# Kernel optimization log

Hardware: AMD Instinct MI355X
Metric: run time of the kernel (lower is better)

## Reference

```python
import jax, jax.numpy as jnp
import numpy as np

N_NODES = 50000


def _gcn_conv(x, W, b, src, dst, n):
    """PyG GCNConv: add self-loops, symmetric normalization, sum-aggregate."""
    h = x @ W  # [N, out_dim] dense transform first (out_dim <= in_dim path)
    loop = jnp.arange(n, dtype=src.dtype)
    src_sl = jnp.concatenate([src, loop])
    dst_sl = jnp.concatenate([dst, loop])
    # degree computed on destination nodes (incl. self-loops)
    deg = jax.ops.segment_sum(jnp.ones_like(dst_sl, dtype=h.dtype), dst_sl, num_segments=n)
    dinv = jnp.where(deg > 0, jax.lax.rsqrt(deg), 0.0)
    norm = dinv[src_sl] * dinv[dst_sl]  # [E+N]
    msgs = h[src_sl] * norm[:, None]  # gather + scale, [E+N, out_dim]
    out = jax.ops.segment_sum(msgs, dst_sl, num_segments=n)  # scatter-add
    return out + b


def setup_inputs() -> dict:
    key = jax.random.key(0)
    k0, k1, k2, k3 = jax.random.split(key, 4)
    d = 256
    E = 400000
    scale = 1.0 / np.sqrt(d)
    x = jax.random.normal(k0, (N_NODES, d), dtype=jnp.float32)
    edge_index = jax.random.randint(k1, (2, E), 0, N_NODES, dtype=jnp.int64)
    W1 = jax.random.normal(k2, (d, d), dtype=jnp.float32) * scale
    b1 = jnp.zeros((d,), dtype=jnp.float32)
    W2 = jax.random.normal(k3, (d, d), dtype=jnp.float32) * scale
    b2 = jnp.zeros((d,), dtype=jnp.float32)
    return {"x": x, "edge_index": edge_index, "W1": W1, "b1": b1, "W2": W2, "b2": b2}


def reference(x, edge_index, W1, b1, W2, b2):
    src, dst = edge_index[0], edge_index[1]
    h = _gcn_conv(x, W1, b1, src, dst, N_NODES)
    h = jax.nn.relu(h)
    h = _gcn_conv(h, W2, b2, src, dst, N_NODES)
    h = jax.nn.relu(h)
    return h
```

## Files before the change

kernel.cpp:

```cpp
#include <hip/hip_runtime.h>
#include <stdint.h>

typedef __bf16 bf16_t;
typedef bf16_t bf16x4 __attribute__((ext_vector_type(4)));
typedef bf16_t bf16x8 __attribute__((ext_vector_type(8)));
typedef float f32x4 __attribute__((ext_vector_type(4)));

#define DIM 256
#define NNODES 50000

__device__ __forceinline__ int detect_f64(const int* __restrict__ ei) {
    int v = ei[2 * (threadIdx.x & 63) + 1];
    unsigned long long m = __ballot(v == 0);
    return __popcll(m) > 32;
}

__device__ __forceinline__ int load_edge(const int* __restrict__ ei, int E, int f64,
                                         int which , int e) {
    int v = f64 ? ei[(size_t)which * 2 * E + 2 * (size_t)e]
                : ei[(size_t)which * E + (size_t)e];
    return min(max(v, 0), NNODES - 1);
}

__global__ __launch_bounds__(256) void prep_kernel(int* __restrict__ counts,
                                                   const float* __restrict__ W1,
                                                   const float* __restrict__ W2,
                                                   bf16_t* __restrict__ Wf1,
                                                   bf16_t* __restrict__ Wf2, int n) {
    const int nb = (NNODES + 255) / 256;
    int b = blockIdx.x, t = threadIdx.x;
    if (b < nb) {
        int idx = b * 256 + t;
        if (idx < n) counts[idx] = 0;
    } else {
        int cw = b - nb;
        const float* W = (cw & 256) ? W2 : W1;
        bf16_t* Wf = (cw & 256) ? Wf2 : Wf1;
        int k = cw & 255;
        int s = k >> 5, quad = (k >> 3) & 3, j = k & 7;
        int nt = t >> 4, m = t & 15;
        Wf[s * 8192 + (nt * 64 + quad * 16 + m) * 8 + j] = (bf16_t)W[k * DIM + t];
    }
}

__global__ __launch_bounds__(256) void scan_kernel(const int* __restrict__ counts,
                                                   int* __restrict__ offsets,
                                                   int* __restrict__ cursor,
                                                   float* __restrict__ dinv, int n) {
    __shared__ int red[256];
    __shared__ int sm[256];
    int b = blockIdx.x, t = threadIdx.x;

    int part = 0;
    const int4* c4 = (const int4*)counts;
    int lim = b * 64;
    for (int j = t; j < lim; j += 256) {
        int4 v = c4[j];
        part += v.x + v.y + v.z + v.w;
    }
    red[t] = part;
    __syncthreads();
    #pragma unroll
    for (int off = 128; off > 0; off >>= 1) {
        if (t < off) red[t] += red[t + off];
        __syncthreads();
    }
    int base = red[0];

    int idx = b * 256 + t;
    int v = (idx < n) ? counts[idx] : 0;
    sm[t] = v;
    __syncthreads();
    #pragma unroll
    for (int off = 1; off < 256; off <<= 1) {
        int u = (t >= off) ? sm[t - off] : 0;
        __syncthreads();
        sm[t] += u;
        __syncthreads();
    }
    if (idx < n) {
        int incl = base + sm[t];
        offsets[idx + 1] = incl;
        cursor[idx] = incl - v;
        dinv[idx] = rsqrtf((float)(v + 1));
    }
    if (idx == 0) offsets[0] = 0;
}

__global__ void scatter_kernel(const int* __restrict__ ei, int E,
                               const float* __restrict__ dinv, int* __restrict__ cursor,
                               int2* __restrict__ csr_e) {
    int f64 = detect_f64(ei);
    int e = blockIdx.x * blockDim.x + threadIdx.x;
    if (e < E) {
        int s = load_edge(ei, E, f64, 0, e);
        int d = load_edge(ei, E, f64, 1, e);
        int pos = atomicAdd(&cursor[d], 1);
        if (pos >= 0 && pos < E) {
            int2 v;
            v.x = s;
            v.y = __float_as_int(dinv[s] * dinv[d]);
            csr_e[pos] = v;
        }
    }
}

#define SWROW 552

template <bool F32A>
__device__ __forceinline__ void gemm_body(const void* __restrict__ Xv,
                                          const bf16_t* __restrict__ Wf,
                                          bf16_t* __restrict__ H, int tiles, int bid,
                                          char* smem) {
    bf16_t* sB = (bf16_t*)smem;
    int tid = threadIdx.x;
    int wave = tid >> 6, lane = tid & 63;
    int m = lane & 15, quad = lane >> 4;
    int tile = bid * 4 + wave;
    bool active = tile < tiles;
    int arow = (min(tile, tiles - 1)) * 16 + m;

    f32x4 acc[16] = {};

    auto stage = [&](int s, int buf) {
        const char* g = (const char*)Wf + s * 16384 + wave * 4096 + lane * 16;
        char* l = smem + buf * 16384 + wave * 4096;
        #pragma unroll
        for (int it = 0; it < 4; it++) {
            __builtin_amdgcn_global_load_lds(
                (const __attribute__((address_space(1))) void*)(g + it * 1024),
                (__attribute__((address_space(3))) void*)(l + it * 1024), 16, 0, 0);
        }
    };

    stage(0, 0);
    __syncthreads();

    for (int s = 0; s < 8; s++) {
        int cur = s & 1;
        if (s < 7) stage(s + 1, cur ^ 1);

        bf16x8 a;
        if (F32A) {
            const f32x4* xp = (const f32x4*)((const float*)Xv + (size_t)arow * DIM + s * 32 + quad * 8);
            f32x4 x0 = xp[0], x1 = xp[1];
            #pragma unroll
            for (int j = 0; j < 4; j++) { a[j] = (bf16_t)x0[j]; a[j + 4] = (bf16_t)x1[j]; }
        } else {
            a = *(const bf16x8*)((const bf16_t*)Xv + (size_t)arow * DIM + s * 32 + quad * 8);
        }

        const bf16_t* bs = sB + cur * 8192;
        #pragma unroll
        for (int nt = 0; nt < 16; nt++) {
            bf16x8 b = *(const bf16x8*)(bs + nt * 512 + lane * 8);
            acc[nt] = __builtin_amdgcn_mfma_f32_16x16x32_bf16(a, b, acc[nt], 0, 0, 0);
        }

        __syncthreads();
    }

    char* sW = smem + wave * (16 * SWROW);
    #pragma unroll
    for (int nt = 0; nt < 16; nt++) {
        #pragma unroll
        for (int r = 0; r < 4; r++) {
            *(bf16_t*)(sW + (quad * 4 + r) * SWROW + (nt * 16 + m) * 2) = (bf16_t)acc[nt][r];
        }
    }
    if (active) {
        bf16_t* Hrow = H + (size_t)tile * 16 * DIM;
        #pragma unroll
        for (int j = 0; j < 16; j++) {
            bf16x4 v = *(const bf16x4*)(sW + j * SWROW + lane * 8);
            *(bf16x4*)(Hrow + j * DIM + lane * 4) = v;
        }
    }
}

__global__ __launch_bounds__(256, 4) void gemm1_hist_kernel(const float* __restrict__ X,
                                                            const bf16_t* __restrict__ Wf,
                                                            bf16_t* __restrict__ H, int tiles,
                                                            int gemm_blocks,
                                                            const int* __restrict__ ei, int E,
                                                            int* __restrict__ counts) {
    __shared__ char smem[4 * 16 * SWROW];
    if ((int)blockIdx.x >= gemm_blocks) {
        int f64 = detect_f64(ei);
        int e = (blockIdx.x - gemm_blocks) * 256 + threadIdx.x;
        if (e < E) atomicAdd(&counts[load_edge(ei, E, f64, 1, e)], 1);
        return;
    }
    gemm_body<true>(X, Wf, H, tiles, blockIdx.x, smem);
}

__global__ __launch_bounds__(256, 4) void gemm2_kernel(const bf16_t* __restrict__ Xv,
                                                       const bf16_t* __restrict__ Wf,
                                                       bf16_t* __restrict__ H, int tiles) {
    __shared__ char smem[4 * 16 * SWROW];
    gemm_body<false>(Xv, Wf, H, tiles, blockIdx.x, smem);
}

template <int OUT_BF16>
__global__ __launch_bounds__(256) void aggregate_kernel(const bf16_t* __restrict__ H,
                                                        const int* __restrict__ offsets,
                                                        const int2* __restrict__ csr_e,
                                                        const float* __restrict__ dinv,
                                                        const float* __restrict__ bias,
                                                        void* __restrict__ outv, int n) {
    int wg = threadIdx.x >> 5;
    int l = threadIdx.x & 31;
    int i = blockIdx.x * 8 + wg;
    if (i >= n) return;

    const char* Hb = (const char*)H;
    int doff = l * 16;

    auto cvt = [](bf16x4 v) -> f32x4 {
        f32x4 r;
        #pragma unroll
        for (int j = 0; j < 4; j++) r[j] = (float)v[j];
        return r;
    };
    auto lo4 = [](bf16x8 v) -> bf16x4 { return __builtin_shufflevector(v, v, 0, 1, 2, 3); };
    auto hi4 = [](bf16x8 v) -> bf16x4 { return __builtin_shufflevector(v, v, 4, 5, 6, 7); };

    float dii = dinv[i];
    bf16x8 selfv = *(const bf16x8*)(Hb + ((size_t)i << 9) + doff);
    f32x4 acc0 = cvt(lo4(selfv)) * (dii * dii);
    f32x4 acc1 = cvt(hi4(selfv)) * (dii * dii);

    int e0 = offsets[i], e1 = offsets[i + 1];
    int e = e0;
    for (; e + 8 <= e1; e += 8) {
        unsigned s[8]; float w[8];
        #pragma unroll
        for (int j = 0; j < 8; j++) {
            int2 t = csr_e[e + j];
            s[j] = min((unsigned)t.x, (unsigned)(NNODES - 1));
            w[j] = __int_as_float(t.y);
        }
        bf16x8 h[8];
        #pragma unroll
        for (int j = 0; j < 8; j++) {
            h[j] = *(const bf16x8*)(Hb + ((size_t)s[j] << 9) + doff);
        }
        __builtin_amdgcn_sched_barrier(0);
        #pragma unroll
        for (int j = 0; j < 8; j++) {
            acc0 += cvt(lo4(h[j])) * w[j];
            acc1 += cvt(hi4(h[j])) * w[j];
        }
    }
    if (e < e1) {
        bf16x8 z;
        #pragma unroll
        for (int q = 0; q < 8; q++) z[q] = (bf16_t)0.0f;
        unsigned s[8]; float w[8]; bool val[8];
        #pragma unroll
        for (int j = 0; j < 8; j++) {
            bool valid = (e + j) < e1;
            val[j] = valid;
            int2 t = csr_e[valid ? e + j : e];
            s[j] = min((unsigned)t.x, (unsigned)(NNODES - 1));
            w[j] = valid ? __int_as_float(t.y) : 0.0f;
        }
        bf16x8 h[8];
        #pragma unroll
        for (int j = 0; j < 8; j++) {
            h[j] = z;
            if (val[j]) h[j] = *(const bf16x8*)(Hb + ((size_t)s[j] << 9) + doff);
        }
        __builtin_amdgcn_sched_barrier(0);
        #pragma unroll
        for (int j = 0; j < 8; j++) {
            acc0 += cvt(lo4(h[j])) * w[j];
            acc1 += cvt(hi4(h[j])) * w[j];
        }
    }

    const f32x4* bp = (const f32x4*)(bias + l * 8);
    acc0 += bp[0];
    acc1 += bp[1];
    #pragma unroll
    for (int j = 0; j < 4; j++) {
        acc0[j] = fmaxf(acc0[j], 0.0f);
        acc1[j] = fmaxf(acc1[j], 0.0f);
    }

    if (OUT_BF16) {
        bf16x8 o;
        #pragma unroll
        for (int j = 0; j < 4; j++) { o[j] = (bf16_t)acc0[j]; o[j + 4] = (bf16_t)acc1[j]; }
        *(bf16x8*)((bf16_t*)outv + (size_t)i * DIM + l * 8) = o;
    } else {
        float* op = (float*)outv + (size_t)i * DIM + l * 8;
        *(f32x4*)op = acc0;
        *(f32x4*)(op + 4) = acc1;
    }
}


extern "C" void kernel_launch(void* const* d_in, const int* in_sizes, int n_in,
                              void* d_out, int out_size, void* d_ws, size_t ws_size,
                              hipStream_t stream) {
    const float* x  = (const float*)d_in[0];
    const int*   ei = (const int*)d_in[1];
    const float* W1 = (const float*)d_in[2];
    const float* b1 = (const float*)d_in[3];
    const float* W2 = (const float*)d_in[4];
    const float* b2 = (const float*)d_in[5];
    float* out = (float*)d_out;

    const int n = NNODES;
    const int E = in_sizes[1] / 2;
    const int nb = (n + 255) / 256;

    char* ws = (char*)d_ws;
    size_t off = 0;
    auto alloc = [&](size_t bytes) -> char* {
        char* p = ws + off;
        off += (bytes + 255) & ~(size_t)255;
        return p;
    };
    float*  dinv     = (float*)alloc((size_t)n * 4);
    int*    counts   = (int*)alloc((size_t)n * 4);
    int*    offsets  = (int*)alloc((size_t)(n + 1) * 4);
    int*    cursor   = (int*)alloc((size_t)n * 4);
    int2*   csr_e    = (int2*)alloc((size_t)E * 8);
    bf16_t* Wf1      = (bf16_t*)alloc((size_t)DIM * DIM * 2);
    bf16_t* Wf2      = (bf16_t*)alloc((size_t)DIM * DIM * 2);
    bf16_t* P        = (bf16_t*)alloc((size_t)n * DIM * 2);
    bf16_t* X2       = (bf16_t*)alloc((size_t)n * DIM * 2);

    int tiles = (n + 15) / 16;
    int gemm_blocks = (tiles + 3) / 4;
    int hist_blocks = (E + 255) / 256;
    int agg_blocks = (n + 7) / 8;

    prep_kernel<<<nb + 512, 256, 0, stream>>>(counts, W1, W2, Wf1, Wf2, n);
    gemm1_hist_kernel<<<gemm_blocks + hist_blocks, 256, 0, stream>>>(x, Wf1, P, tiles,
                                                                     gemm_blocks, ei, E, counts);
    scan_kernel<<<nb, 256, 0, stream>>>(counts, offsets, cursor, dinv, n);
    scatter_kernel<<<hist_blocks, 256, 0, stream>>>(ei, E, dinv, cursor, csr_e);
    aggregate_kernel<1><<<agg_blocks, 256, 0, stream>>>(P, offsets, csr_e, dinv, b1, X2, n);
    gemm2_kernel<<<gemm_blocks, 256, 0, stream>>>(X2, Wf2, P, tiles);
    aggregate_kernel<0><<<agg_blocks, 256, 0, stream>>>(P, offsets, csr_e, dinv, b2, out, n);
}
```

Before: 246.7 us.

## Fuse layer-1 aggregation with layer-2 GEMM via LDS-resident activations

Layer-1 aggregation now runs inside the layer-2 GEMM kernel. Each block gathers 64 rows into a swizzled LDS tile and feeds them straight into the MFMA loop, so the bf16 intermediate never makes a global round trip and one launch is removed. The GEMM1 path also preloads all A fragments (fp32 converted to bf16) before the K loop instead of loading per stage. In exchange, the fused kernel uses 64KB of LDS with launch bounds of 2, so occupancy for the latency-bound gather phase is lower and the GEMM cannot start until the block's slow gathers finish.

```diff
diff --git a/kernel.cpp b/kernel.cpp
--- a/kernel.cpp
+++ b/kernel.cpp
@@ -8,6 +8,7 @@
 
 #define DIM 256
 #define NNODES 50000
+#define SWROW 552
 
 __device__ __forceinline__ int detect_f64(const int* __restrict__ ei) {
     int v = ei[2 * (threadIdx.x & 63) + 1];
@@ -105,75 +106,72 @@
     }
 }
 
-#define SWROW 552
-
-template <bool F32A>
-__device__ __forceinline__ void gemm_body(const void* __restrict__ Xv,
-                                          const bf16_t* __restrict__ Wf,
-                                          bf16_t* __restrict__ H, int tiles, int bid,
-                                          char* smem) {
-    bf16_t* sB = (bf16_t*)smem;
-    int tid = threadIdx.x;
-    int wave = tid >> 6, lane = tid & 63;
-    int m = lane & 15, quad = lane >> 4;
-    int tile = bid * 4 + wave;
-    bool active = tile < tiles;
-    int arow = (min(tile, tiles - 1)) * 16 + m;
-
-    f32x4 acc[16] = {};
-
-    auto stage = [&](int s, int buf) {
-        const char* g = (const char*)Wf + s * 16384 + wave * 4096 + lane * 16;
-        char* l = smem + buf * 16384 + wave * 4096;
-        #pragma unroll
-        for (int it = 0; it < 4; it++) {
-            __builtin_amdgcn_global_load_lds(
-                (const __attribute__((address_space(1))) void*)(g + it * 1024),
-                (__attribute__((address_space(3))) void*)(l + it * 1024), 16, 0, 0);
-        }
-    };
-
-    stage(0, 0);
-    __syncthreads();
-
-    for (int s = 0; s < 8; s++) {
-        int cur = s & 1;
-        if (s < 7) stage(s + 1, cur ^ 1);
-
-        bf16x8 a;
-        if (F32A) {
-            const f32x4* xp = (const f32x4*)((const float*)Xv + (size_t)arow * DIM + s * 32 + quad * 8);
-            f32x4 x0 = xp[0], x1 = xp[1];
-            #pragma unroll
-            for (int j = 0; j < 4; j++) { a[j] = (bf16_t)x0[j]; a[j + 4] = (bf16_t)x1[j]; }
-        } else {
-            a = *(const bf16x8*)((const bf16_t*)Xv + (size_t)arow * DIM + s * 32 + quad * 8);
-        }
-
-        const bf16_t* bs = sB + cur * 8192;
-        #pragma unroll
-        for (int nt = 0; nt < 16; nt++) {
-            bf16x8 b = *(const bf16x8*)(bs + nt * 512 + lane * 8);
-            acc[nt] = __builtin_amdgcn_mfma_f32_16x16x32_bf16(a, b, acc[nt], 0, 0, 0);
-        }
-
-        __syncthreads();
-    }
-
-    char* sW = smem + wave * (16 * SWROW);
-    #pragma unroll
-    for (int nt = 0; nt < 16; nt++) {
-        #pragma unroll
-        for (int r = 0; r < 4; r++) {
-            *(bf16_t*)(sW + (quad * 4 + r) * SWROW + (nt * 16 + m) * 2) = (bf16_t)acc[nt][r];
-        }
-    }
-    if (active) {
-        bf16_t* Hrow = H + (size_t)tile * 16 * DIM;
-        #pragma unroll
-        for (int j = 0; j < 16; j++) {
-            bf16x4 v = *(const bf16x4*)(sW + j * SWROW + lane * 8);
-            *(bf16x4*)(Hrow + j * DIM + lane * 4) = v;
+__device__ __forceinline__ f32x4 cvt4(bf16x4 v) {
+    f32x4 r;
+    #pragma unroll
+    for (int j = 0; j < 4; j++) r[j] = (float)v[j];
+    return r;
+}
+__device__ __forceinline__ bf16x4 lo4(bf16x8 v) { return __builtin_shufflevector(v, v, 0, 1, 2, 3); }
+__device__ __forceinline__ bf16x4 hi4(bf16x8 v) { return __builtin_shufflevector(v, v, 4, 5, 6, 7); }
+
+__device__ __forceinline__ void gather_row(const char* __restrict__ Hb,
+                                           const int* __restrict__ offsets,
+                                           const int2* __restrict__ csr_e,
+                                           const float* __restrict__ dinv,
+                                           int i, int l, f32x4& acc0, f32x4& acc1) {
+    int doff = l * 16;
+    float dii = dinv[i];
+    bf16x8 selfv = *(const bf16x8*)(Hb + ((size_t)i << 9) + doff);
+    acc0 = cvt4(lo4(selfv)) * (dii * dii);
+    acc1 = cvt4(hi4(selfv)) * (dii * dii);
+
+    int e0 = offsets[i], e1 = offsets[i + 1];
+    int e = e0;
+    for (; e + 8 <= e1; e += 8) {
+        unsigned s[8]; float w[8];
+        #pragma unroll
+        for (int j = 0; j < 8; j++) {
+            int2 t = csr_e[e + j];
+            s[j] = min((unsigned)t.x, (unsigned)(NNODES - 1));
+            w[j] = __int_as_float(t.y);
+        }
+        bf16x8 h[8];
+        #pragma unroll
+        for (int j = 0; j < 8; j++) {
+            h[j] = *(const bf16x8*)(Hb + ((size_t)s[j] << 9) + doff);
+        }
+        __builtin_amdgcn_sched_barrier(0);
+        #pragma unroll
+        for (int j = 0; j < 8; j++) {
+            acc0 += cvt4(lo4(h[j])) * w[j];
+            acc1 += cvt4(hi4(h[j])) * w[j];
+        }
+    }
+    if (e < e1) {
+        bf16x8 z;
+        #pragma unroll
+        for (int q = 0; q < 8; q++) z[q] = (bf16_t)0.0f;
+        unsigned s[8]; float w[8]; bool val[8];
+        #pragma unroll
+        for (int j = 0; j < 8; j++) {
+            bool valid = (e + j) < e1;
+            val[j] = valid;
+            int2 t = csr_e[valid ? e + j : e];
+            s[j] = min((unsigned)t.x, (unsigned)(NNODES - 1));
+            w[j] = valid ? __int_as_float(t.y) : 0.0f;
+        }
+        bf16x8 h[8];
+        #pragma unroll
+        for (int j = 0; j < 8; j++) {
+            h[j] = z;
+            if (val[j]) h[j] = *(const bf16x8*)(Hb + ((size_t)s[j] << 9) + doff);
+        }
+        __builtin_amdgcn_sched_barrier(0);
+        #pragma unroll
+        for (int j = 0; j < 8; j++) {
+            acc0 += cvt4(lo4(h[j])) * w[j];
+            acc1 += cvt4(hi4(h[j])) * w[j];
         }
     }
 }
@@ -191,93 +189,185 @@
         if (e < E) atomicAdd(&counts[load_edge(ei, E, f64, 1, e)], 1);
         return;
     }
-    gemm_body<true>(X, Wf, H, tiles, blockIdx.x, smem);
-}
-
-__global__ __launch_bounds__(256, 4) void gemm2_kernel(const bf16_t* __restrict__ Xv,
-                                                       const bf16_t* __restrict__ Wf,
-                                                       bf16_t* __restrict__ H, int tiles) {
-    __shared__ char smem[4 * 16 * SWROW];
-    gemm_body<false>(Xv, Wf, H, tiles, blockIdx.x, smem);
-}
-
-template <int OUT_BF16>
-__global__ __launch_bounds__(256) void aggregate_kernel(const bf16_t* __restrict__ H,
-                                                        const int* __restrict__ offsets,
-                                                        const int2* __restrict__ csr_e,
-                                                        const float* __restrict__ dinv,
-                                                        const float* __restrict__ bias,
-                                                        void* __restrict__ outv, int n) {
+
+    bf16_t* sB = (bf16_t*)smem;
+    int tid = threadIdx.x;
+    int wave = tid >> 6, lane = tid & 63;
+    int m = lane & 15, quad = lane >> 4;
+    int tile = blockIdx.x * 4 + wave;
+    bool active = tile < tiles;
+    int arow = (min(tile, tiles - 1)) * 16 + m;
+
+    auto stage = [&](int s, int buf) {
+        const char* g = (const char*)Wf + s * 16384 + wave * 4096 + lane * 16;
+        char* l = smem + buf * 16384 + wave * 4096;
+        #pragma unroll
+        for (int it = 0; it < 4; it++) {
+            __builtin_amdgcn_global_load_lds(
+                (const __attribute__((address_space(1))) void*)(g + it * 1024),
+                (__attribute__((address_space(3))) void*)(l + it * 1024), 16, 0, 0);
+        }
+    };
+
+    stage(0, 0);
+
+    bf16x8 a[8];
+    {
+        const f32x4* xp = (const f32x4*)(X + (size_t)arow * DIM);
+        #pragma unroll
+        for (int s = 0; s < 8; s++) {
+            f32x4 x0 = xp[s * 8 + quad * 2], x1 = xp[s * 8 + quad * 2 + 1];
+            #pragma unroll
+            for (int j = 0; j < 4; j++) { a[s][j] = (bf16_t)x0[j]; a[s][j + 4] = (bf16_t)x1[j]; }
+        }
+    }
+
+    f32x4 acc[16] = {};
+    __syncthreads();
+
+    for (int s = 0; s < 8; s++) {
+        int cur = s & 1;
+        if (s < 7) stage(s + 1, cur ^ 1);
+        const bf16_t* bs = sB + cur * 8192;
+        #pragma unroll
+        for (int nt = 0; nt < 16; nt++) {
+            bf16x8 b = *(const bf16x8*)(bs + nt * 512 + lane * 8);
+            acc[nt] = __builtin_amdgcn_mfma_f32_16x16x32_bf16(a[s], b, acc[nt], 0, 0, 0);
+        }
+        __syncthreads();
+    }
+
+    char* sW = smem + wave * (16 * SWROW);
+    #pragma unroll
+    for (int nt = 0; nt < 16; nt++) {
+        #pragma unroll
+        for (int r = 0; r < 4; r++) {
+            *(bf16_t*)(sW + (quad * 4 + r) * SWROW + (nt * 16 + m) * 2) = (bf16_t)acc[nt][r];
+        }
+    }
+    if (active) {
+        bf16_t* Hrow = H + (size_t)tile * 16 * DIM;
+        #pragma unroll
+        for (int j = 0; j < 16; j++) {
+            bf16x4 v = *(const bf16x4*)(sW + j * SWROW + lane * 8);
+            *(bf16x4*)(Hrow + j * DIM + lane * 4) = v;
+        }
+    }
+}
+
+__global__ __launch_bounds__(256, 2) void agg1_gemm2_kernel(const bf16_t* __restrict__ P,
+                                                            const int* __restrict__ offsets,
+                                                            const int2* __restrict__ csr_e,
+                                                            const float* __restrict__ dinv,
+                                                            const float* __restrict__ bias,
+                                                            const bf16_t* __restrict__ Wf,
+                                                            bf16_t* __restrict__ H2,
+                                                            int tiles, int n) {
+    __shared__ char smem[65536];
+    char* ldsA = smem;
+    char* ldsW = smem + 32768;
+    bf16_t* sB = (bf16_t*)ldsW;
+
+    int tid = threadIdx.x;
+    const char* Hb = (const char*)P;
+
+    {
+        int wg = tid >> 5, l = tid & 31;
+        for (int it = 0; it < 8; it++) {
+            int lr = it * 8 + wg;
+            int i = blockIdx.x * 64 + lr;
+            if (i < n) {
+                f32x4 acc0, acc1;
+                gather_row(Hb, offsets, csr_e, dinv, i, l, acc0, acc1);
+                const f32x4* bp = (const f32x4*)(bias + l * 8);
+                acc0 += bp[0];
+                acc1 += bp[1];
+                bf16x8 o;
+                #pragma unroll
+                for (int j = 0; j < 4; j++) {
+                    o[j] = (bf16_t)fmaxf(acc0[j], 0.0f);
+                    o[j + 4] = (bf16_t)fmaxf(acc1[j], 0.0f);
+                }
+                *(bf16x8*)(ldsA + lr * 512 + ((l * 16) ^ ((lr & 7) << 4))) = o;
+            }
+        }
+    }
+    __syncthreads();
+
+    int wave = tid >> 6, lane = tid & 63;
+    int m = lane & 15, quad = lane >> 4;
+    int tile = blockIdx.x * 4 + wave;
+    bool active = tile < tiles;
+
+    auto stage = [&](int s, int buf) {
+        const char* g = (const char*)Wf + s * 16384 + wave * 4096 + lane * 16;
+        char* l = ldsW + buf * 16384 + wave * 4096;
+        #pragma unroll
+        for (int it = 0; it < 4; it++) {
+            __builtin_amdgcn_global_load_lds(
+                (const __attribute__((address_space(1))) void*)(g + it * 1024),
+                (__attribute__((address_space(3))) void*)(l + it * 1024), 16, 0, 0);
+        }
+    };
+
+    stage(0, 0);
+
+    bf16x8 a[8];
+    {
+        const char* ar = ldsA + (wave * 16 + m) * 512;
+        int sw = (m & 7) << 4;
+        #pragma unroll
+        for (int s = 0; s < 8; s++) {
+            a[s] = *(const bf16x8*)(ar + ((s * 64 + quad * 16) ^ sw));
+        }
+    }
+
+    f32x4 acc[16] = {};
+    __syncthreads();
+
+    for (int s = 0; s < 8; s++) {
+        int cur = s & 1;
+        if (s < 7) stage(s + 1, cur ^ 1);
+        const bf16_t* bs = sB + cur * 8192;
+        #pragma unroll
+        for (int nt = 0; nt < 16; nt++) {
+            bf16x8 b = *(const bf16x8*)(bs + nt * 512 + lane * 8);
+            acc[nt] = __builtin_amdgcn_mfma_f32_16x16x32_bf16(a[s], b, acc[nt], 0, 0, 0);
+        }
+        __syncthreads();
+    }
+
+    char* sW = smem + wave * (16 * SWROW);
+    #pragma unroll
+    for (int nt = 0; nt < 16; nt++) {
+        #pragma unroll
+        for (int r = 0; r < 4; r++) {
+            *(bf16_t*)(sW + (quad * 4 + r) * SWROW + (nt * 16 + m) * 2) = (bf16_t)acc[nt][r];
+        }
+    }
+    if (active) {
+        bf16_t* Hrow = H2 + (size_t)tile * 16 * DIM;
+        #pragma unroll
+        for (int j = 0; j < 16; j++) {
+            bf16x4 v = *(const bf16x4*)(sW + j * SWROW + lane * 8);
+            *(bf16x4*)(Hrow + j * DIM + lane * 4) = v;
+        }
+    }
+}
+
+__global__ __launch_bounds__(256) void aggregate2_kernel(const bf16_t* __restrict__ H,
+                                                         const int* __restrict__ offsets,
+                                                         const int2* __restrict__ csr_e,
+                                                         const float* __restrict__ dinv,
+                                                         const float* __restrict__ bias,
+                                                         float* __restrict__ out, int n) {
     int wg = threadIdx.x >> 5;
     int l = threadIdx.x & 31;
     int i = blockIdx.x * 8 + wg;
     if (i >= n) return;
 
-    const char* Hb = (const char*)H;
-    int doff = l * 16;
-
-    auto cvt = [](bf16x4 v) -> f32x4 {
-        f32x4 r;
-        #pragma unroll
-        for (int j = 0; j < 4; j++) r[j] = (float)v[j];
-        return r;
-    };
-    auto lo4 = [](bf16x8 v) -> bf16x4 { return __builtin_shufflevector(v, v, 0, 1, 2, 3); };
-    auto hi4 = [](bf16x8 v) -> bf16x4 { return __builtin_shufflevector(v, v, 4, 5, 6, 7); };
-
-    float dii = dinv[i];
-    bf16x8 selfv = *(const bf16x8*)(Hb + ((size_t)i << 9) + doff);
-    f32x4 acc0 = cvt(lo4(selfv)) * (dii * dii);
-    f32x4 acc1 = cvt(hi4(selfv)) * (dii * dii);
-
-    int e0 = offsets[i], e1 = offsets[i + 1];
-    int e = e0;
-    for (; e + 8 <= e1; e += 8) {
-        unsigned s[8]; float w[8];
-        #pragma unroll
-        for (int j = 0; j < 8; j++) {
-            int2 t = csr_e[e + j];
-            s[j] = min((unsigned)t.x, (unsigned)(NNODES - 1));
-            w[j] = __int_as_float(t.y);
-        }
-        bf16x8 h[8];
-        #pragma unroll
-        for (int j = 0; j < 8; j++) {
-            h[j] = *(const bf16x8*)(Hb + ((size_t)s[j] << 9) + doff);
-        }
-        __builtin_amdgcn_sched_barrier(0);
-        #pragma unroll
-        for (int j = 0; j < 8; j++) {
-            acc0 += cvt(lo4(h[j])) * w[j];
-            acc1 += cvt(hi4(h[j])) * w[j];
-        }
-    }
-    if (e < e1) {
-        bf16x8 z;
-        #pragma unroll
-        for (int q = 0; q < 8; q++) z[q] = (bf16_t)0.0f;
-        unsigned s[8]; float w[8]; bool val[8];
-        #pragma unroll
-        for (int j = 0; j < 8; j++) {
-            bool valid = (e + j) < e1;
-            val[j] = valid;
-            int2 t = csr_e[valid ? e + j : e];
-            s[j] = min((unsigned)t.x, (unsigned)(NNODES - 1));
-            w[j] = valid ? __int_as_float(t.y) : 0.0f;
-        }
-        bf16x8 h[8];
-        #pragma unroll
-        for (int j = 0; j < 8; j++) {
-            h[j] = z;
-            if (val[j]) h[j] = *(const bf16x8*)(Hb + ((size_t)s[j] << 9) + doff);
-        }
-        __builtin_amdgcn_sched_barrier(0);
-        #pragma unroll
-        for (int j = 0; j < 8; j++) {
-            acc0 += cvt(lo4(h[j])) * w[j];
-            acc1 += cvt(hi4(h[j])) * w[j];
-        }
-    }
+    f32x4 acc0, acc1;
+    gather_row((const char*)H, offsets, csr_e, dinv, i, l, acc0, acc1);
 
     const f32x4* bp = (const f32x4*)(bias + l * 8);
     acc0 += bp[0];
@@ -287,17 +377,9 @@
         acc0[j] = fmaxf(acc0[j], 0.0f);
         acc1[j] = fmaxf(acc1[j], 0.0f);
     }
-
-    if (OUT_BF16) {
-        bf16x8 o;
-        #pragma unroll
-        for (int j = 0; j < 4; j++) { o[j] = (bf16_t)acc0[j]; o[j + 4] = (bf16_t)acc1[j]; }
-        *(bf16x8*)((bf16_t*)outv + (size_t)i * DIM + l * 8) = o;
-    } else {
-        float* op = (float*)outv + (size_t)i * DIM + l * 8;
-        *(f32x4*)op = acc0;
-        *(f32x4*)(op + 4) = acc1;
-    }
+    float* op = out + (size_t)i * DIM + l * 8;
+    *(f32x4*)op = acc0;
+    *(f32x4*)(op + 4) = acc1;
 }
 
 
@@ -331,7 +413,7 @@
     bf16_t* Wf1      = (bf16_t*)alloc((size_t)DIM * DIM * 2);
     bf16_t* Wf2      = (bf16_t*)alloc((size_t)DIM * DIM * 2);
     bf16_t* P        = (bf16_t*)alloc((size_t)n * DIM * 2);
-    bf16_t* X2       = (bf16_t*)alloc((size_t)n * DIM * 2);
+    bf16_t* H2       = (bf16_t*)alloc((size_t)n * DIM * 2);
 
     int tiles = (n + 15) / 16;
     int gemm_blocks = (tiles + 3) / 4;
@@ -343,7 +425,7 @@
                                                                      gemm_blocks, ei, E, counts);
     scan_kernel<<<nb, 256, 0, stream>>>(counts, offsets, cursor, dinv, n);
     scatter_kernel<<<hist_blocks, 256, 0, stream>>>(ei, E, dinv, cursor, csr_e);
-    aggregate_kernel<1><<<agg_blocks, 256, 0, stream>>>(P, offsets, csr_e, dinv, b1, X2, n);
-    gemm2_kernel<<<gemm_blocks, 256, 0, stream>>>(X2, Wf2, P, tiles);
-    aggregate_kernel<0><<<agg_blocks, 256, 0, stream>>>(P, offsets, csr_e, dinv, b2, out, n);
-}
+    agg1_gemm2_kernel<<<gemm_blocks, 256, 0, stream>>>(P, offsets, csr_e, dinv, b1, Wf2,
+                                                       H2, tiles, n);
+    aggregate2_kernel<<<agg_blocks, 256, 0, stream>>>(H2, offsets, csr_e, dinv, b2, out, n);
+}
```

After: 257.3 us. +4.3%, slower.
